# Optimization experiments

Hardware: AMD Instinct MI355X
Metric: run time of the kernel (lower is better)

The kernel has to match this reference:

```python
import jax, jax.numpy as jnp
import numpy as np

C = 1024
FACTOR = 4
C_INT = C * FACTOR


def setup_inputs() -> dict:
    key = jax.random.key(0)
    ks = jax.random.split(key, 6)
    act = jax.random.normal(ks[0], (4, 2048, C), dtype=jnp.float32)
    mask = jnp.ones((4, 2048), dtype=jnp.float32)
    # LayerNorm params
    ln_scale = jnp.ones((C,), dtype=jnp.float32)
    ln_bias = jnp.zeros((C,), dtype=jnp.float32)
    # Linear 1 (init='linear'): lecun-normal-ish
    w1 = jax.random.normal(ks[1], (C, C_INT), dtype=jnp.float32) / np.sqrt(C)
    b1 = jnp.zeros((C_INT,), dtype=jnp.float32)
    # Linear 2 (init='final' -> zeros in AF2; use small random so grads are nontrivial)
    w2 = jax.random.normal(ks[2], (C_INT, C), dtype=jnp.float32) * 0.02
    b2 = jnp.zeros((C,), dtype=jnp.float32)
    return {"act": act, "mask": mask, "ln_scale": ln_scale, "ln_bias": ln_bias,
            "w1": w1, "b1": b1, "w2": w2, "b2": b2}


def _layernorm(x, scale, bias, eps=1e-5):
    mu = jnp.mean(x, axis=-1, keepdims=True)
    var = jnp.mean(jnp.square(x - mu), axis=-1, keepdims=True)
    return (x - mu) * jax.lax.rsqrt(var + eps) * scale + bias


def reference(act, mask, ln_scale, ln_bias, w1, b1, w2, b2):
    # mask is accepted but unused, matching the original forward.
    x = _layernorm(act, ln_scale, ln_bias)
    h = jax.nn.relu(jnp.einsum('bsc,cf->bsf', x, w1) + b1)
    return jnp.einsum('bsf,fc->bsc', h, w2) + b2
```

## Files before the change

kernel.cpp:

```cpp
#include <hip/hip_runtime.h>
#include <hip/hip_bf16.h>
#include <cstdint>

typedef unsigned short u16;
typedef __bf16 bf16x8 __attribute__((ext_vector_type(8)));
typedef float floatx4 __attribute__((ext_vector_type(4)));

#define AS1 __attribute__((address_space(1)))
#define AS3 __attribute__((address_space(3)))

#define SCHED0  __builtin_amdgcn_sched_barrier(0)
#define BARRIER __builtin_amdgcn_s_barrier()

static __device__ __forceinline__ u16 f2bf(float f) {
    union { float f; unsigned int u; } v; v.f = f;
    unsigned int u = v.u;
    return (u16)((u + 0x7FFFu + ((u >> 16) & 1u)) >> 16);
}

static __device__ __forceinline__ unsigned lds_off(const u16* p) {
    return (unsigned)(unsigned long long)(const AS3 u16*)p;
}
static __device__ __forceinline__ bf16x8 ds_read8(unsigned off) {
    bf16x8 r;
    asm volatile("ds_read_b128 %0, %1" : "=&v"(r) : "v"(off));
    return r;
}

template <int N> __device__ __forceinline__ void wvm() {
    if constexpr (N == 0) asm volatile("s_waitcnt vmcnt(0)" ::: "memory");
    else if constexpr (N == 3) asm volatile("s_waitcnt vmcnt(3)" ::: "memory");
    else if constexpr (N == 6) asm volatile("s_waitcnt vmcnt(6)" ::: "memory");
}
template <int N> __device__ __forceinline__ void wlg() {
    if constexpr (N == 0) asm volatile("s_waitcnt lgkmcnt(0)" ::: "memory");
    else if constexpr (N == 4) asm volatile("s_waitcnt lgkmcnt(4)" ::: "memory");
    else if constexpr (N == 8) asm volatile("s_waitcnt lgkmcnt(8)" ::: "memory");
}

__device__ __forceinline__ void transpose_body(
    const float* __restrict__ in, u16* __restrict__ out,
    int R, int Ccols, int bx, int by, int tid, float (*tile)[33])
{
    const int r0 = by * 128, c0 = bx * 32;
#pragma unroll
    for (int p = 0; p < 4; ++p) {
        const int f = p * 256 + tid;
        const int r = f >> 3, c4 = (f & 7) * 4;
        const float4 v = *(const float4*)&in[(size_t)(r0 + r) * Ccols + c0 + c4];
        tile[r][c4 + 0] = v.x; tile[r][c4 + 1] = v.y;
        tile[r][c4 + 2] = v.z; tile[r][c4 + 3] = v.w;
    }
    __syncthreads();
    const int wv = tid >> 6, ln = tid & 63;
#pragma unroll
    for (int i = 0; i < 8; ++i) {
        const int c = i * 4 + wv;
        ushort2 o = { f2bf(tile[ln * 2][c]), f2bf(tile[ln * 2 + 1][c]) };
        *(ushort2*)&out[(size_t)(c0 + c) * R + r0 + ln * 2] = o;
    }
}

__global__ __launch_bounds__(256)
void prep(const float* __restrict__ w1, const float* __restrict__ w2,
          const float* __restrict__ act, const float* __restrict__ ln_scale,
          const float* __restrict__ ln_bias,
          u16* __restrict__ W1t, u16* __restrict__ W2t, u16* __restrict__ X)
{
    __shared__ float tile[128][33];
    const int id  = blockIdx.x;
    const int tid = threadIdx.x;

    if (id < 1024) {
        transpose_body(w1, W1t, 1024, 4096, id & 127, id >> 7, tid, tile);
        return;
    }
    if (id < 2048) {
        const int t = id - 1024;
        transpose_body(w2, W2t, 4096, 1024, t & 31, t >> 5, tid, tile);
        return;
    }
    const int row = id - 2048;
    const float4 v = ((const float4*)(act + (size_t)row * 1024))[tid];
    float s  = v.x + v.y + v.z + v.w;
    float ss = v.x * v.x + v.y * v.y + v.z * v.z + v.w * v.w;
#pragma unroll
    for (int off = 32; off > 0; off >>= 1) {
        s  += __shfl_xor(s, off, 64);
        ss += __shfl_xor(ss, off, 64);
    }
    float* red = &tile[0][0];
    const int wave = tid >> 6, lane = tid & 63;
    if (lane == 0) { red[wave] = s; red[4 + wave] = ss; }
    __syncthreads();
    s  = red[0] + red[1] + red[2] + red[3];
    ss = red[4] + red[5] + red[6] + red[7];
    const float mu  = s * (1.0f / 1024.0f);
    const float var = ss * (1.0f / 1024.0f) - mu * mu;
    const float rs  = rsqrtf(var + 1e-5f);
    const float4 sc = ((const float4*)ln_scale)[tid];
    const float4 bi = ((const float4*)ln_bias)[tid];
    ushort4 o;
    o.x = f2bf((v.x - mu) * rs * sc.x + bi.x);
    o.y = f2bf((v.y - mu) * rs * sc.y + bi.y);
    o.z = f2bf((v.z - mu) * rs * sc.z + bi.z);
    o.w = f2bf((v.w - mu) * rs * sc.w + bi.w);
    ((ushort4*)(X + (size_t)row * 1024))[tid] = o;
}

__global__ __launch_bounds__(512, 2)
void gemm1(const u16* __restrict__ A, const u16* __restrict__ Bt,
           const float* __restrict__ bias, u16* __restrict__ H)
{
    constexpr int K = 1024, N = 4096;
    constexpr int ASZ = 256 * 64;
    __shared__ __align__(16) u16 Alds[2 * ASZ];
    __shared__ __align__(16) u16 Blds[2 * ASZ];

    const int tid  = threadIdx.x;
    const int wave = tid >> 6;
    const int lane = tid & 63;
    const int srow = lane >> 3;
    const int sst  = lane & 7;
    const int quad = lane >> 4;
    const int l16  = lane & 15;
    const int rkey = l16 & 7;
    const int wm   = wave >> 2;
    const int wn   = wave & 3;

    const int id = blockIdx.x;
    const int bm = id & 31;
    const int bn = id >> 5;

    const u16* Ag = A  + (size_t)bm * 256 * K;
    const u16* Bg = Bt + (size_t)bn * 256 * K;

    auto stA = [&](int buf, int c, int k0) {
        const int row = c * 64 + wave * 8 + srow;
        const int col = (sst ^ (row & 7)) * 8;
        __builtin_amdgcn_global_load_lds(
            (AS1 void*)(Ag + (size_t)row * K + k0 + col),
            (AS3 void*)(&Alds[buf * ASZ + c * 4096 + wave * 512]), 16, 0, 0);
    };
    auto stB = [&](int buf, int c, int k0) {
        const int row = c * 64 + wave * 8 + srow;
        const int col = (sst ^ (row & 7)) * 8;
        __builtin_amdgcn_global_load_lds(
            (AS1 void*)(Bg + (size_t)row * K + k0 + col),
            (AS3 void*)(&Blds[buf * ASZ + c * 4096 + wave * 512]), 16, 0, 0);
    };

    const unsigned Abase = lds_off(&Alds[0]);
    const unsigned Bbase = lds_off(&Blds[0]);
    unsigned aoff[8][2], boff[4][2];
#pragma unroll
    for (int mi = 0; mi < 8; ++mi)
#pragma unroll
        for (int kh = 0; kh < 2; ++kh)
            aoff[mi][kh] = ((wm * 128 + mi * 16 + l16) * 64 +
                            ((kh * 4 + quad) ^ rkey) * 8) * 2;
#pragma unroll
    for (int ni = 0; ni < 4; ++ni)
#pragma unroll
        for (int kh = 0; kh < 2; ++kh)
            boff[ni][kh] = ((wn * 64 + ni * 16 + l16) * 64 +
                            ((kh * 4 + quad) ^ rkey) * 8) * 2;

    floatx4 acc[8][4];
#pragma unroll
    for (int i = 0; i < 8; ++i)
#pragma unroll
        for (int j = 0; j < 4; ++j)
            acc[i][j] = (floatx4){0.f, 0.f, 0.f, 0.f};

    constexpr int NT = K / 64;

    stA(0, 0, 0); stA(0, 2, 0); stA(0, 1, 0); stA(0, 3, 0);
    stB(0, 0, 0); stB(0, 1, 0); stB(0, 2, 0); stB(0, 3, 0);
    wvm<0>();
    SCHED0; BARRIER; SCHED0;

    bf16x8 afrX[4], afrY[4], bres0[4], bres1[4];
#pragma unroll
    for (int j = 0; j < 4; ++j) afrX[j] = ds_read8(Abase + aoff[j][0]);
#pragma unroll
    for (int ni = 0; ni < 4; ++ni) bres0[ni] = ds_read8(Bbase + boff[ni][0]);

    for (int t = 0; t < NT; ++t) {
        const int cur = t & 1, nb = cur ^ 1;
        const unsigned ab0 = Abase + (unsigned)(cur * ASZ * 2);
        const unsigned bb0 = Bbase + (unsigned)(cur * ASZ * 2);
        const unsigned abn = Abase + (unsigned)(nb * ASZ * 2);
        const unsigned bbn = Bbase + (unsigned)(nb * ASZ * 2);
        const int k1 = (t + 1) * 64;
        const bool st = (t + 1 < NT);

#pragma unroll
        for (int j = 0; j < 4; ++j) afrY[j] = ds_read8(ab0 + aoff[4 + j][0]);
#pragma unroll
        for (int ni = 0; ni < 4; ++ni) bres1[ni] = ds_read8(bb0 + boff[ni][1]);
        if (st) { stA(nb, 0, k1); stA(nb, 2, k1); stA(nb, 1, k1); stA(nb, 3, k1); }
        wlg<8>();
        SCHED0;
        __builtin_amdgcn_s_setprio(1);
#pragma unroll
        for (int j = 0; j < 4; ++j)
#pragma unroll
            for (int ni = 0; ni < 4; ++ni)
                acc[j][ni] = __builtin_amdgcn_mfma_f32_16x16x32_bf16(
                    bres0[ni], afrX[j], acc[j][ni], 0, 0, 0);
        __builtin_amdgcn_s_setprio(0);
        SCHED0; BARRIER; SCHED0;

#pragma unroll
        for (int j = 0; j < 4; ++j) afrX[j] = ds_read8(ab0 + aoff[j][1]);
        if (st) { stB(nb, 0, k1); stB(nb, 1, k1); stB(nb, 2, k1); stB(nb, 3, k1); }
        wlg<8>();
        SCHED0;
        __builtin_amdgcn_s_setprio(1);
#pragma unroll
        for (int j = 0; j < 4; ++j)
#pragma unroll
            for (int ni = 0; ni < 4; ++ni)
                acc[4 + j][ni] = __builtin_amdgcn_mfma_f32_16x16x32_bf16(
                    bres0[ni], afrY[j], acc[4 + j][ni], 0, 0, 0);
        __builtin_amdgcn_s_setprio(0);
        SCHED0; BARRIER; SCHED0;

#pragma unroll
        for (int j = 0; j < 4; ++j) afrY[j] = ds_read8(ab0 + aoff[4 + j][1]);
        wlg<4>();
        SCHED0;
        __builtin_amdgcn_s_setprio(1);
#pragma unroll
        for (int j = 0; j < 4; ++j)
#pragma unroll
            for (int ni = 0; ni < 4; ++ni)
                acc[j][ni] = __builtin_amdgcn_mfma_f32_16x16x32_bf16(
                    bres1[ni], afrX[j], acc[j][ni], 0, 0, 0);
        __builtin_amdgcn_s_setprio(0);
        SCHED0;
        if (st) wvm<0>();
        BARRIER; SCHED0;

        if (st) {
#pragma unroll
            for (int j = 0; j < 4; ++j) afrX[j] = ds_read8(abn + aoff[j][0]);
#pragma unroll
            for (int ni = 0; ni < 4; ++ni) bres0[ni] = ds_read8(bbn + boff[ni][0]);
            wlg<8>();
        } else wlg<0>();
        SCHED0;
        __builtin_amdgcn_s_setprio(1);
#pragma unroll
        for (int j = 0; j < 4; ++j)
#pragma unroll
            for (int ni = 0; ni < 4; ++ni)
                acc[4 + j][ni] = __builtin_amdgcn_mfma_f32_16x16x32_bf16(
                    bres1[ni], afrY[j], acc[4 + j][ni], 0, 0, 0);
        __builtin_amdgcn_s_setprio(0);
        SCHED0; BARRIER; SCHED0;
    }

    const int mbase = bm * 256 + wm * 128;
    const int nbase = bn * 256 + wn * 64;
#pragma unroll
    for (int mi = 0; mi < 8; ++mi) {
        const int m = mbase + mi * 16 + l16;
#pragma unroll
        for (int ni = 0; ni < 4; ++ni) {
            const int n0 = nbase + ni * 16 + quad * 4;
            const float4 bv = *(const float4*)&bias[n0];
            float v0 = fmaxf(acc[mi][ni][0] + bv.x, 0.f);
            float v1 = fmaxf(acc[mi][ni][1] + bv.y, 0.f);
            float v2 = fmaxf(acc[mi][ni][2] + bv.z, 0.f);
            float v3 = fmaxf(acc[mi][ni][3] + bv.w, 0.f);
            ushort4 o = { f2bf(v0), f2bf(v1), f2bf(v2), f2bf(v3) };
            *(ushort4*)&H[(size_t)m * N + n0] = o;
        }
    }
}

__global__ __launch_bounds__(512, 2)
void gemm2(const u16* __restrict__ A, const u16* __restrict__ Bt,
           const float* __restrict__ bias, float* __restrict__ Cout)
{
    constexpr int K = 4096, N = 1024;
    constexpr int ASZ = 2 * 256 * 32;
    constexpr int BSZ = 2 * 128 * 32;
    __shared__ __align__(16) u16 Alds[3 * ASZ];
    __shared__ __align__(16) u16 Blds[3 * BSZ];

    const int tid  = threadIdx.x;
    const int wave = tid >> 6;
    const int lane = tid & 63;
    const int quad = lane >> 4;
    const int l16  = lane & 15;
    const int key4 = (l16 >> 1) & 3;
    const int wm   = wave >> 1;
    const int wn   = wave & 1;

    const int id = blockIdx.x;
    const int bm = id & 31;
    const int bn = id >> 5;

    const u16* Ag = A  + (size_t)bm * 256 * K;
    const u16* Bg = Bt + (size_t)bn * 128 * K;

    auto stA = [&](int buf, int kh, int c, int k0) {
        const int row = c * 128 + wave * 16 + (lane >> 2);
        const int col = kh * 32 + ((lane & 3) ^ ((row >> 1) & 3)) * 8;
        __builtin_amdgcn_global_load_lds(
            (AS1 void*)(Ag + (size_t)row * K + k0 + col),
            (AS3 void*)(&Alds[buf * ASZ + kh * 8192 + c * 4096 + wave * 512]),
            16, 0, 0);
    };
    auto stB = [&](int buf, int kh, int k0) {
        const int row = wave * 16 + (lane >> 2);
        const int col = kh * 32 + ((lane & 3) ^ ((row >> 1) & 3)) * 8;
        __builtin_amdgcn_global_load_lds(
            (AS1 void*)(Bg + (size_t)row * K + k0 + col),
            (AS3 void*)(&Blds[buf * BSZ + kh * 4096 + wave * 512]), 16, 0, 0);
    };

    const unsigned Ab = lds_off(&Alds[0]);
    const unsigned Bb = lds_off(&Blds[0]);
    unsigned aoff[4], boff[4];
#pragma unroll
    for (int mi = 0; mi < 4; ++mi)
        aoff[mi] = ((wm * 64 + mi * 16 + l16) * 32 + (quad ^ key4) * 8) * 2;
#pragma unroll
    for (int ni = 0; ni < 4; ++ni)
        boff[ni] = ((wn * 64 + ni * 16 + l16) * 32 + (quad ^ key4) * 8) * 2;

    floatx4 acc[4][4];
#pragma unroll
    for (int i = 0; i < 4; ++i)
#pragma unroll
        for (int j = 0; j < 4; ++j)
            acc[i][j] = (floatx4){0.f, 0.f, 0.f, 0.f};

    constexpr int NT = K / 64;

    stA(0, 0, 0, 0);  stA(0, 0, 1, 0);  stB(0, 0, 0);
    stA(0, 1, 0, 0);  stA(0, 1, 1, 0);  stB(0, 1, 0);
    stA(1, 0, 0, 64); stA(1, 0, 1, 64); stB(1, 0, 64);
    stA(1, 1, 0, 64); stA(1, 1, 1, 64); stB(1, 1, 64);
    wvm<6>();
    SCHED0; BARRIER; SCHED0;

    bf16x8 fa[2][4], fb[2][4];
#pragma unroll
    for (int i = 0; i < 4; ++i) {
        fa[0][i] = ds_read8(Ab + aoff[i]);
        fb[0][i] = ds_read8(Bb + boff[i]);
    }

    int bs0 = 0, bs1 = 1, bs2 = 2;
    for (int t = 0; t < NT; ++t) {
        const int k2 = (t + 2) * 64;
        const bool st  = (t + 2 < NT);
        const bool rd1 = (t + 1 < NT);
        const unsigned a0 = Ab + (unsigned)(bs0 * ASZ * 2);
        const unsigned b0 = Bb + (unsigned)(bs0 * BSZ * 2);
        const unsigned a1 = Ab + (unsigned)(bs1 * ASZ * 2);
        const unsigned b1 = Bb + (unsigned)(bs1 * BSZ * 2);

#pragma unroll
        for (int i = 0; i < 4; ++i) {
            fa[1][i] = ds_read8(a0 + 16384u + aoff[i]);
            fb[1][i] = ds_read8(b0 + 8192u  + boff[i]);
        }
        if (st) { stA(bs2, 0, 0, k2); stA(bs2, 0, 1, k2); stB(bs2, 0, k2); }
        wlg<8>();
        SCHED0;
        __builtin_amdgcn_s_setprio(1);
#pragma unroll
        for (int mi = 0; mi < 4; ++mi)
#pragma unroll
            for (int ni = 0; ni < 4; ++ni)
                acc[mi][ni] = __builtin_amdgcn_mfma_f32_16x16x32_bf16(
                    fb[0][ni], fa[0][mi], acc[mi][ni], 0, 0, 0);
        __builtin_amdgcn_s_setprio(0);
        SCHED0;
        if (st)       wvm<6>();
        else if (rd1) wvm<3>();
        BARRIER; SCHED0;

        if (rd1) {
#pragma unroll
            for (int i = 0; i < 4; ++i) {
                fa[0][i] = ds_read8(a1 + aoff[i]);
                fb[0][i] = ds_read8(b1 + boff[i]);
            }
        }
        if (st) { stA(bs2, 1, 0, k2); stA(bs2, 1, 1, k2); stB(bs2, 1, k2); }
        if (rd1) wlg<8>(); else wlg<0>();
        SCHED0;
        __builtin_amdgcn_s_setprio(1);
#pragma unroll
        for (int mi = 0; mi < 4; ++mi)
#pragma unroll
            for (int ni = 0; ni < 4; ++ni)
                acc[mi][ni] = __builtin_amdgcn_mfma_f32_16x16x32_bf16(
                    fb[1][ni], fa[1][mi], acc[mi][ni], 0, 0, 0);
        __builtin_amdgcn_s_setprio(0);
        SCHED0;
        if (st)       wvm<6>();
        else if (rd1) wvm<0>();
        BARRIER; SCHED0;

        const int tmp = bs0; bs0 = bs1; bs1 = bs2; bs2 = tmp;
    }

    const int mbase = bm * 256 + wm * 64;
    const int nbase = bn * 128 + wn * 64;
#pragma unroll
    for (int mi = 0; mi < 4; ++mi) {
        const int m = mbase + mi * 16 + l16;
#pragma unroll
        for (int ni = 0; ni < 4; ++ni) {
            const int n0 = nbase + ni * 16 + quad * 4;
            const float4 bv = *(const float4*)&bias[n0];
            float4 o = { acc[mi][ni][0] + bv.x, acc[mi][ni][1] + bv.y,
                         acc[mi][ni][2] + bv.z, acc[mi][ni][3] + bv.w };
            *(float4*)&Cout[(size_t)m * N + n0] = o;
        }
    }
}

extern "C" void kernel_launch(void* const* d_in, const int* in_sizes, int n_in,
                              void* d_out, int out_size, void* d_ws, size_t ws_size,
                              hipStream_t stream)
{
    const float* act      = (const float*)d_in[0];
    const float* ln_scale = (const float*)d_in[2];
    const float* ln_bias  = (const float*)d_in[3];
    const float* w1       = (const float*)d_in[4];
    const float* b1       = (const float*)d_in[5];
    const float* w2       = (const float*)d_in[6];
    const float* b2       = (const float*)d_in[7];
    float* out = (float*)d_out;

    const int M = 8192, C = 1024, CI = 4096;

    u16* X   = (u16*)d_ws;
    u16* W1t = X   + (size_t)M * C;
    u16* W2t = W1t + (size_t)CI * C;
    u16* H   = W2t + (size_t)C * CI;

    prep<<<10240, 256, 0, stream>>>(w1, w2, act, ln_scale, ln_bias, W1t, W2t, X);
    gemm1<<<(M / 256) * (CI / 256), 512, 0, stream>>>(X, W1t, b1, H);
    gemm2<<<(M / 256) * (C / 128), 512, 0, stream>>>(H, W2t, b2, out);
}
```

Before: 248.8 us.

## Restructure gemm1 into 4-stage K=32 LDS pipeline with deeper prefetch

Replaces the double-buffered K=64 tile loop in gemm1 with a four-buffer ring of K=32 tiles. Loads run three tiles ahead, and the waits become partial vmcnt waits instead of draining every load. Register fragments ping-pong between two sets across an unrolled pair of iterations, and the LDS swizzle changes to fit 32-element rows. The aim is to hide global-memory latency better and cut full vmcnt(0) stalls, at the cost of twice as many barriers per unit of K and more complex wait counting.

```diff
diff --git a/kernel.cpp b/kernel.cpp
--- a/kernel.cpp
+++ b/kernel.cpp
@@ -30,7 +30,9 @@
 template <int N> __device__ __forceinline__ void wvm() {
     if constexpr (N == 0) asm volatile("s_waitcnt vmcnt(0)" ::: "memory");
     else if constexpr (N == 3) asm volatile("s_waitcnt vmcnt(3)" ::: "memory");
+    else if constexpr (N == 4) asm volatile("s_waitcnt vmcnt(4)" ::: "memory");
     else if constexpr (N == 6) asm volatile("s_waitcnt vmcnt(6)" ::: "memory");
+    else if constexpr (N == 8) asm volatile("s_waitcnt vmcnt(8)" ::: "memory");
 }
 template <int N> __device__ __forceinline__ void wlg() {
     if constexpr (N == 0) asm volatile("s_waitcnt lgkmcnt(0)" ::: "memory");
@@ -112,19 +114,17 @@
 void gemm1(const u16* __restrict__ A, const u16* __restrict__ Bt,
            const float* __restrict__ bias, u16* __restrict__ H)
 {
-    constexpr int K = 1024, N = 4096;
-    constexpr int ASZ = 256 * 64;
-    __shared__ __align__(16) u16 Alds[2 * ASZ];
-    __shared__ __align__(16) u16 Blds[2 * ASZ];
+    constexpr int K = 1024, N = 4096, NT = 32;
+    constexpr int ABUF = 256 * 32;
+    __shared__ __align__(16) u16 Alds[4 * ABUF];
+    __shared__ __align__(16) u16 Blds[4 * ABUF];
 
     const int tid  = threadIdx.x;
     const int wave = tid >> 6;
     const int lane = tid & 63;
-    const int srow = lane >> 3;
-    const int sst  = lane & 7;
     const int quad = lane >> 4;
     const int l16  = lane & 15;
-    const int rkey = l16 & 7;
+    const int key4 = (l16 >> 1) & 3;
     const int wm   = wave >> 2;
     const int wn   = wave & 3;
 
@@ -135,36 +135,30 @@
     const u16* Ag = A  + (size_t)bm * 256 * K;
     const u16* Bg = Bt + (size_t)bn * 256 * K;
 
-    auto stA = [&](int buf, int c, int k0) {
-        const int row = c * 64 + wave * 8 + srow;
-        const int col = (sst ^ (row & 7)) * 8;
+    auto stA = [&](int buf, int i, int kt) {
+        const int row = i * 128 + wave * 16 + (lane >> 2);
+        const int col = ((lane & 3) ^ ((row >> 1) & 3)) * 8;
         __builtin_amdgcn_global_load_lds(
-            (AS1 void*)(Ag + (size_t)row * K + k0 + col),
-            (AS3 void*)(&Alds[buf * ASZ + c * 4096 + wave * 512]), 16, 0, 0);
+            (AS1 void*)(Ag + (size_t)row * K + kt * 32 + col),
+            (AS3 void*)(&Alds[buf * ABUF + i * 4096 + wave * 512]), 16, 0, 0);
     };
-    auto stB = [&](int buf, int c, int k0) {
-        const int row = c * 64 + wave * 8 + srow;
-        const int col = (sst ^ (row & 7)) * 8;
+    auto stB = [&](int buf, int i, int kt) {
+        const int row = i * 128 + wave * 16 + (lane >> 2);
+        const int col = ((lane & 3) ^ ((row >> 1) & 3)) * 8;
         __builtin_amdgcn_global_load_lds(
-            (AS1 void*)(Bg + (size_t)row * K + k0 + col),
-            (AS3 void*)(&Blds[buf * ASZ + c * 4096 + wave * 512]), 16, 0, 0);
+            (AS1 void*)(Bg + (size_t)row * K + kt * 32 + col),
+            (AS3 void*)(&Blds[buf * ABUF + i * 4096 + wave * 512]), 16, 0, 0);
     };
 
-    const unsigned Abase = lds_off(&Alds[0]);
-    const unsigned Bbase = lds_off(&Blds[0]);
-    unsigned aoff[8][2], boff[4][2];
+    const unsigned Ab = lds_off(&Alds[0]);
+    const unsigned Bb = lds_off(&Blds[0]);
+    unsigned aoff[8], boff[4];
 #pragma unroll
     for (int mi = 0; mi < 8; ++mi)
-#pragma unroll
-        for (int kh = 0; kh < 2; ++kh)
-            aoff[mi][kh] = ((wm * 128 + mi * 16 + l16) * 64 +
-                            ((kh * 4 + quad) ^ rkey) * 8) * 2;
+        aoff[mi] = ((wm * 128 + mi * 16 + l16) * 32 + (quad ^ key4) * 8) * 2;
 #pragma unroll
     for (int ni = 0; ni < 4; ++ni)
-#pragma unroll
-        for (int kh = 0; kh < 2; ++kh)
-            boff[ni][kh] = ((wn * 64 + ni * 16 + l16) * 64 +
-                            ((kh * 4 + quad) ^ rkey) * 8) * 2;
+        boff[ni] = ((wn * 64 + ni * 16 + l16) * 32 + (quad ^ key4) * 8) * 2;
 
     floatx4 acc[8][4];
 #pragma unroll
@@ -173,94 +167,70 @@
         for (int j = 0; j < 4; ++j)
             acc[i][j] = (floatx4){0.f, 0.f, 0.f, 0.f};
 
-    constexpr int NT = K / 64;
-
-    stA(0, 0, 0); stA(0, 2, 0); stA(0, 1, 0); stA(0, 3, 0);
-    stB(0, 0, 0); stB(0, 1, 0); stB(0, 2, 0); stB(0, 3, 0);
-    wvm<0>();
+    stA(0, 0, 0); stA(0, 1, 0);  stB(0, 0, 0); stB(0, 1, 0);
+    stA(1, 0, 1); stA(1, 1, 1);  stB(1, 0, 1); stB(1, 1, 1);
+    stA(2, 0, 2); stA(2, 1, 2);  stB(2, 0, 2); stB(2, 1, 2);
+    wvm<8>();
     SCHED0; BARRIER; SCHED0;
 
-    bf16x8 afrX[4], afrY[4], bres0[4], bres1[4];
-#pragma unroll
-    for (int j = 0; j < 4; ++j) afrX[j] = ds_read8(Abase + aoff[j][0]);
-#pragma unroll
-    for (int ni = 0; ni < 4; ++ni) bres0[ni] = ds_read8(Bbase + boff[ni][0]);
-
-    for (int t = 0; t < NT; ++t) {
-        const int cur = t & 1, nb = cur ^ 1;
-        const unsigned ab0 = Abase + (unsigned)(cur * ASZ * 2);
-        const unsigned bb0 = Bbase + (unsigned)(cur * ASZ * 2);
-        const unsigned abn = Abase + (unsigned)(nb * ASZ * 2);
-        const unsigned bbn = Bbase + (unsigned)(nb * ASZ * 2);
-        const int k1 = (t + 1) * 64;
-        const bool st = (t + 1 < NT);
-
-#pragma unroll
-        for (int j = 0; j < 4; ++j) afrY[j] = ds_read8(ab0 + aoff[4 + j][0]);
-#pragma unroll
-        for (int ni = 0; ni < 4; ++ni) bres1[ni] = ds_read8(bb0 + boff[ni][1]);
-        if (st) { stA(nb, 0, k1); stA(nb, 2, k1); stA(nb, 1, k1); stA(nb, 3, k1); }
-        wlg<8>();
-        SCHED0;
-        __builtin_amdgcn_s_setprio(1);
-#pragma unroll
-        for (int j = 0; j < 4; ++j)
-#pragma unroll
-            for (int ni = 0; ni < 4; ++ni)
-                acc[j][ni] = __builtin_amdgcn_mfma_f32_16x16x32_bf16(
-                    bres0[ni], afrX[j], acc[j][ni], 0, 0, 0);
-        __builtin_amdgcn_s_setprio(0);
-        SCHED0; BARRIER; SCHED0;
-
-#pragma unroll
-        for (int j = 0; j < 4; ++j) afrX[j] = ds_read8(ab0 + aoff[j][1]);
-        if (st) { stB(nb, 0, k1); stB(nb, 1, k1); stB(nb, 2, k1); stB(nb, 3, k1); }
-        wlg<8>();
-        SCHED0;
-        __builtin_amdgcn_s_setprio(1);
-#pragma unroll
-        for (int j = 0; j < 4; ++j)
-#pragma unroll
-            for (int ni = 0; ni < 4; ++ni)
-                acc[4 + j][ni] = __builtin_amdgcn_mfma_f32_16x16x32_bf16(
-                    bres0[ni], afrY[j], acc[4 + j][ni], 0, 0, 0);
-        __builtin_amdgcn_s_setprio(0);
-        SCHED0; BARRIER; SCHED0;
-
-#pragma unroll
-        for (int j = 0; j < 4; ++j) afrY[j] = ds_read8(ab0 + aoff[4 + j][1]);
-        wlg<4>();
-        SCHED0;
-        __builtin_amdgcn_s_setprio(1);
-#pragma unroll
-        for (int j = 0; j < 4; ++j)
-#pragma unroll
-            for (int ni = 0; ni < 4; ++ni)
-                acc[j][ni] = __builtin_amdgcn_mfma_f32_16x16x32_bf16(
-                    bres1[ni], afrX[j], acc[j][ni], 0, 0, 0);
-        __builtin_amdgcn_s_setprio(0);
-        SCHED0;
-        if (st) wvm<0>();
-        BARRIER; SCHED0;
-
-        if (st) {
-#pragma unroll
-            for (int j = 0; j < 4; ++j) afrX[j] = ds_read8(abn + aoff[j][0]);
-#pragma unroll
-            for (int ni = 0; ni < 4; ++ni) bres0[ni] = ds_read8(bbn + boff[ni][0]);
-            wlg<8>();
-        } else wlg<0>();
-        SCHED0;
-        __builtin_amdgcn_s_setprio(1);
-#pragma unroll
-        for (int j = 0; j < 4; ++j)
-#pragma unroll
-            for (int ni = 0; ni < 4; ++ni)
-                acc[4 + j][ni] = __builtin_amdgcn_mfma_f32_16x16x32_bf16(
-                    bres1[ni], afrY[j], acc[4 + j][ni], 0, 0, 0);
-        __builtin_amdgcn_s_setprio(0);
-        SCHED0; BARRIER; SCHED0;
-    }
+    bf16x8 a03A[4], a03B[4], bresA[4], bresB[4], a47[4];
+#pragma unroll
+    for (int j = 0; j < 4; ++j) a03A[j] = ds_read8(Ab + aoff[j]);
+#pragma unroll
+    for (int n = 0; n < 4; ++n) bresA[n] = ds_read8(Bb + boff[n]);
+
+#define PHASES(t, cA, cB, nA, nB)                                             \
+    do {                                                                      \
+        const unsigned abc = Ab + (unsigned)(((t) & 3) * 16384);              \
+        const unsigned abn = Ab + (unsigned)((((t) + 1) & 3) * 16384);        \
+        const unsigned bbn = Bb + (unsigned)((((t) + 1) & 3) * 16384);        \
+                                                           \
+        _Pragma("unroll")                                                     \
+        for (int j = 0; j < 4; ++j) a47[j] = ds_read8(abc + aoff[4 + j]);     \
+        if ((t) + 3 < NT) { stA(((t) + 3) & 3, 0, (t) + 3);                   \
+                            stA(((t) + 3) & 3, 1, (t) + 3); }                 \
+        wlg<4>();                                                             \
+        SCHED0;                                                               \
+        __builtin_amdgcn_s_setprio(1);                                        \
+        _Pragma("unroll")                                                     \
+        for (int j = 0; j < 4; ++j)                                           \
+            _Pragma("unroll")                                                 \
+            for (int n = 0; n < 4; ++n)                                       \
+                acc[j][n] = __builtin_amdgcn_mfma_f32_16x16x32_bf16(          \
+                    cB[n], cA[j], acc[j][n], 0, 0, 0);                        \
+        __builtin_amdgcn_s_setprio(0);                                        \
+        SCHED0;                                                               \
+        if ((t) + 3 < NT)      wvm<6>();                                      \
+        else if ((t) + 2 < NT) wvm<4>();                                      \
+        else if ((t) + 1 < NT) wvm<0>();                                      \
+        BARRIER; SCHED0;                                                      \
+                                                           \
+        if ((t) + 1 < NT) {                                                   \
+            _Pragma("unroll")                                                 \
+            for (int j = 0; j < 4; ++j) nA[j] = ds_read8(abn + aoff[j]);      \
+            _Pragma("unroll")                                                 \
+            for (int n = 0; n < 4; ++n) nB[n] = ds_read8(bbn + boff[n]);      \
+        }                                                                     \
+        if ((t) + 3 < NT) { stB(((t) + 3) & 3, 0, (t) + 3);                   \
+                            stB(((t) + 3) & 3, 1, (t) + 3); }                 \
+        if ((t) + 1 < NT) wlg<8>(); else wlg<0>();                            \
+        SCHED0;                                                               \
+        __builtin_amdgcn_s_setprio(1);                                        \
+        _Pragma("unroll")                                                     \
+        for (int j = 0; j < 4; ++j)                                           \
+            _Pragma("unroll")                                                 \
+            for (int n = 0; n < 4; ++n)                                       \
+                acc[4 + j][n] = __builtin_amdgcn_mfma_f32_16x16x32_bf16(      \
+                    cB[n], a47[j], acc[4 + j][n], 0, 0, 0);                   \
+        __builtin_amdgcn_s_setprio(0);                                        \
+        SCHED0; BARRIER; SCHED0;                                              \
+    } while (0)
+
+    for (int tp = 0; tp < NT; tp += 2) {
+        PHASES(tp,     a03A, bresA, a03B, bresB);
+        PHASES(tp + 1, a03B, bresB, a03A, bresA);
+    }
+#undef PHASES
 
     const int mbase = bm * 256 + wm * 128;
     const int nbase = bn * 256 + wn * 64;
```

Result: slower. 260.9 us (+4.9%).

## Triple-buffer B tiles in gemm1 and restructure the K-loop schedule

Applied to the files above, without the earlier changes.

Adds a third LDS buffer for the B operand so B tiles are prefetched two K-steps ahead while A stays double-buffered, with rotating buffer indices and vmcnt(4) partial waits. The loop body is rewritten into four phases that each issue LDS reads, hit a barrier, wait for lgkmcnt(0), then run 16 MFMAs. The old version overlapped the next phase's reads with the current MFMAs. The aim is to hide global-load latency for B, at the cost of more LDS (which may threaten 2 blocks per CU) and a full LDS wait in every phase.

```diff
diff --git a/kernel.cpp b/kernel.cpp
--- a/kernel.cpp
+++ b/kernel.cpp
@@ -30,11 +30,11 @@
 template <int N> __device__ __forceinline__ void wvm() {
     if constexpr (N == 0) asm volatile("s_waitcnt vmcnt(0)" ::: "memory");
     else if constexpr (N == 3) asm volatile("s_waitcnt vmcnt(3)" ::: "memory");
+    else if constexpr (N == 4) asm volatile("s_waitcnt vmcnt(4)" ::: "memory");
     else if constexpr (N == 6) asm volatile("s_waitcnt vmcnt(6)" ::: "memory");
 }
 template <int N> __device__ __forceinline__ void wlg() {
     if constexpr (N == 0) asm volatile("s_waitcnt lgkmcnt(0)" ::: "memory");
-    else if constexpr (N == 4) asm volatile("s_waitcnt lgkmcnt(4)" ::: "memory");
     else if constexpr (N == 8) asm volatile("s_waitcnt lgkmcnt(8)" ::: "memory");
 }
 
@@ -112,10 +112,10 @@
 void gemm1(const u16* __restrict__ A, const u16* __restrict__ Bt,
            const float* __restrict__ bias, u16* __restrict__ H)
 {
-    constexpr int K = 1024, N = 4096;
+    constexpr int K = 1024, N = 4096, NT = 16;
     constexpr int ASZ = 256 * 64;
     __shared__ __align__(16) u16 Alds[2 * ASZ];
-    __shared__ __align__(16) u16 Blds[2 * ASZ];
+    __shared__ __align__(16) u16 Blds[3 * ASZ];
 
     const int tid  = threadIdx.x;
     const int wave = tid >> 6;
@@ -173,93 +173,93 @@
         for (int j = 0; j < 4; ++j)
             acc[i][j] = (floatx4){0.f, 0.f, 0.f, 0.f};
 
-    constexpr int NT = K / 64;
-
     stA(0, 0, 0); stA(0, 2, 0); stA(0, 1, 0); stA(0, 3, 0);
     stB(0, 0, 0); stB(0, 1, 0); stB(0, 2, 0); stB(0, 3, 0);
-    wvm<0>();
+    stB(1, 0, 64); stB(1, 1, 64); stB(1, 2, 64); stB(1, 3, 64);
+    wvm<4>();
     SCHED0; BARRIER; SCHED0;
 
-    bf16x8 afrX[4], afrY[4], bres0[4], bres1[4];
-#pragma unroll
-    for (int j = 0; j < 4; ++j) afrX[j] = ds_read8(Abase + aoff[j][0]);
-#pragma unroll
-    for (int ni = 0; ni < 4; ++ni) bres0[ni] = ds_read8(Bbase + boff[ni][0]);
-
+    bf16x8 afr[4], bfr[4];
+    int b0 = 0, b1 = 1, b2 = 2;
     for (int t = 0; t < NT; ++t) {
-        const int cur = t & 1, nb = cur ^ 1;
-        const unsigned ab0 = Abase + (unsigned)(cur * ASZ * 2);
-        const unsigned bb0 = Bbase + (unsigned)(cur * ASZ * 2);
-        const unsigned abn = Abase + (unsigned)(nb * ASZ * 2);
-        const unsigned bbn = Bbase + (unsigned)(nb * ASZ * 2);
+        const unsigned abc = Abase + (unsigned)((t & 1) * ASZ * 2);
+        const unsigned bbc = Bbase + (unsigned)(b0 * ASZ * 2);
+        const int nbA = (t + 1) & 1;
         const int k1 = (t + 1) * 64;
-        const bool st = (t + 1 < NT);
-
-#pragma unroll
-        for (int j = 0; j < 4; ++j) afrY[j] = ds_read8(ab0 + aoff[4 + j][0]);
-#pragma unroll
-        for (int ni = 0; ni < 4; ++ni) bres1[ni] = ds_read8(bb0 + boff[ni][1]);
-        if (st) { stA(nb, 0, k1); stA(nb, 2, k1); stA(nb, 1, k1); stA(nb, 3, k1); }
-        wlg<8>();
-        SCHED0;
-        __builtin_amdgcn_s_setprio(1);
-#pragma unroll
-        for (int j = 0; j < 4; ++j)
-#pragma unroll
-            for (int ni = 0; ni < 4; ++ni)
-                acc[j][ni] = __builtin_amdgcn_mfma_f32_16x16x32_bf16(
-                    bres0[ni], afrX[j], acc[j][ni], 0, 0, 0);
+        const int k2 = (t + 2) * 64;
+
+#pragma unroll
+        for (int j = 0; j < 4; ++j) afr[j] = ds_read8(abc + aoff[j][0]);
+#pragma unroll
+        for (int n = 0; n < 4; ++n) bfr[n] = ds_read8(bbc + boff[n][0]);
+        if (t + 1 < NT) { stA(nbA, 0, k1); stA(nbA, 2, k1);
+                          stA(nbA, 1, k1); stA(nbA, 3, k1); }
+        SCHED0; BARRIER;
+        wlg<0>();
+        SCHED0;
+        __builtin_amdgcn_s_setprio(1);
+#pragma unroll
+        for (int j = 0; j < 4; ++j)
+#pragma unroll
+            for (int n = 0; n < 4; ++n)
+                acc[j][n] = __builtin_amdgcn_mfma_f32_16x16x32_bf16(
+                    bfr[n], afr[j], acc[j][n], 0, 0, 0);
         __builtin_amdgcn_s_setprio(0);
         SCHED0; BARRIER; SCHED0;
 
 #pragma unroll
-        for (int j = 0; j < 4; ++j) afrX[j] = ds_read8(ab0 + aoff[j][1]);
-        if (st) { stB(nb, 0, k1); stB(nb, 1, k1); stB(nb, 2, k1); stB(nb, 3, k1); }
-        wlg<8>();
-        SCHED0;
-        __builtin_amdgcn_s_setprio(1);
-#pragma unroll
-        for (int j = 0; j < 4; ++j)
-#pragma unroll
-            for (int ni = 0; ni < 4; ++ni)
-                acc[4 + j][ni] = __builtin_amdgcn_mfma_f32_16x16x32_bf16(
-                    bres0[ni], afrY[j], acc[4 + j][ni], 0, 0, 0);
+        for (int j = 0; j < 4; ++j) afr[j] = ds_read8(abc + aoff[4 + j][0]);
+        if (t + 2 < NT) { stB(b2, 0, k2); stB(b2, 1, k2);
+                          stB(b2, 2, k2); stB(b2, 3, k2); }
+        SCHED0; BARRIER;
+        wlg<0>();
+        SCHED0;
+        __builtin_amdgcn_s_setprio(1);
+#pragma unroll
+        for (int j = 0; j < 4; ++j)
+#pragma unroll
+            for (int n = 0; n < 4; ++n)
+                acc[4 + j][n] = __builtin_amdgcn_mfma_f32_16x16x32_bf16(
+                    bfr[n], afr[j], acc[4 + j][n], 0, 0, 0);
         __builtin_amdgcn_s_setprio(0);
         SCHED0; BARRIER; SCHED0;
 
 #pragma unroll
-        for (int j = 0; j < 4; ++j) afrY[j] = ds_read8(ab0 + aoff[4 + j][1]);
-        wlg<4>();
-        SCHED0;
-        __builtin_amdgcn_s_setprio(1);
-#pragma unroll
-        for (int j = 0; j < 4; ++j)
-#pragma unroll
-            for (int ni = 0; ni < 4; ++ni)
-                acc[j][ni] = __builtin_amdgcn_mfma_f32_16x16x32_bf16(
-                    bres1[ni], afrX[j], acc[j][ni], 0, 0, 0);
-        __builtin_amdgcn_s_setprio(0);
-        SCHED0;
-        if (st) wvm<0>();
+        for (int j = 0; j < 4; ++j) afr[j] = ds_read8(abc + aoff[j][1]);
+#pragma unroll
+        for (int n = 0; n < 4; ++n) bfr[n] = ds_read8(bbc + boff[n][1]);
+        SCHED0; BARRIER;
+        wlg<0>();
+        SCHED0;
+        __builtin_amdgcn_s_setprio(1);
+#pragma unroll
+        for (int j = 0; j < 4; ++j)
+#pragma unroll
+            for (int n = 0; n < 4; ++n)
+                acc[j][n] = __builtin_amdgcn_mfma_f32_16x16x32_bf16(
+                    bfr[n], afr[j], acc[j][n], 0, 0, 0);
+        __builtin_amdgcn_s_setprio(0);
+        SCHED0; BARRIER; SCHED0;
+
+#pragma unroll
+        for (int j = 0; j < 4; ++j) afr[j] = ds_read8(abc + aoff[4 + j][1]);
+        SCHED0; BARRIER;
+        wlg<0>();
+        SCHED0;
+        __builtin_amdgcn_s_setprio(1);
+#pragma unroll
+        for (int j = 0; j < 4; ++j)
+#pragma unroll
+            for (int n = 0; n < 4; ++n)
+                acc[4 + j][n] = __builtin_amdgcn_mfma_f32_16x16x32_bf16(
+                    bfr[n], afr[j], acc[4 + j][n], 0, 0, 0);
+        __builtin_amdgcn_s_setprio(0);
+        SCHED0;
+        if (t + 2 < NT)      wvm<4>();
+        else if (t + 1 < NT) wvm<0>();
         BARRIER; SCHED0;
 
-        if (st) {
-#pragma unroll
-            for (int j = 0; j < 4; ++j) afrX[j] = ds_read8(abn + aoff[j][0]);
-#pragma unroll
-            for (int ni = 0; ni < 4; ++ni) bres0[ni] = ds_read8(bbn + boff[ni][0]);
-            wlg<8>();
-        } else wlg<0>();
-        SCHED0;
-        __builtin_amdgcn_s_setprio(1);
-#pragma unroll
-        for (int j = 0; j < 4; ++j)
-#pragma unroll
-            for (int ni = 0; ni < 4; ++ni)
-                acc[4 + j][ni] = __builtin_amdgcn_mfma_f32_16x16x32_bf16(
-                    bres1[ni], afrY[j], acc[4 + j][ni], 0, 0, 0);
-        __builtin_amdgcn_s_setprio(0);
-        SCHED0; BARRIER; SCHED0;
+        const int tmp = b0; b0 = b1; b1 = b2; b2 = tmp;
     }
 
     const int mbase = bm * 256 + wm * 128;
```

New measurement: 257.7 us. 1.04x slower.
